# Kernel optimization log

Measured on AMD Instinct MI355X. Metric: run time of the kernel, lower is better.

Reference implementation:

```python
import jax, jax.numpy as jnp
import numpy as np

B, T, H, NH, L = 16, 1024, 256, 2, 2
NH = 4
FF = 4 * H
DT = 0.1


def _ln(x, g, b, eps=1e-5):
    m = x.mean(-1, keepdims=True)
    v = ((x - m) ** 2).mean(-1, keepdims=True)
    return (x - m) * jax.lax.rsqrt(v + eps) * g + b


def setup_inputs() -> dict:
    key = jax.random.key(0)
    ks = jax.random.split(key, 16)
    def g(i, shape, s=0.05):
        return jax.random.normal(ks[i], shape, jnp.float32) * s
    return {
        "x": jax.random.normal(ks[0], (B, T, 1), jnp.float32),
        # input projection: Linear(1->H) + LayerNorm
        "W_in": g(1, (H, 1), 0.5), "b_in": jnp.zeros(H, jnp.float32),
        "ln_in_g": jnp.ones(H, jnp.float32), "ln_in_b": jnp.zeros(H, jnp.float32),
        # LiquidODECell
        "W_x": g(2, (H, H)), "b_x": jnp.zeros(H, jnp.float32),
        "tau": jnp.ones(H, jnp.float32), "W_rec": g(3, (H, H)),
        # transformer layers (stacked over L)
        "Wqkv": g(4, (L, 3 * H, H)), "bqkv": jnp.zeros((L, 3 * H), jnp.float32),
        "Wo": g(5, (L, H, H)), "bo": jnp.zeros((L, H), jnp.float32),
        "ln1_g": jnp.ones((L, H), jnp.float32), "ln1_b": jnp.zeros((L, H), jnp.float32),
        "W1": g(6, (L, FF, H)), "b1": jnp.zeros((L, FF), jnp.float32),
        "W2": g(7, (L, H, FF)), "b2": jnp.zeros((L, H), jnp.float32),
        "ln2_g": jnp.ones((L, H), jnp.float32), "ln2_b": jnp.zeros((L, H), jnp.float32),
        # output head
        "W_fc": g(8, (1, H)), "b_fc": jnp.zeros(1, jnp.float32),
    }


def reference(x, W_in, b_in, ln_in_g, ln_in_b, W_x, b_x, tau, W_rec,
              Wqkv, bqkv, Wo, bo, ln1_g, ln1_b, W1, b1, W2, b2, ln2_g, ln2_b,
              W_fc, b_fc):
    # input proj: Linear -> LayerNorm -> GELU (exact erf gelu, matches nn.GELU)
    u = jax.nn.gelu(_ln(x @ W_in.T + b_in, ln_in_g, ln_in_b), approximate=False)  # (B,T,H)
    # LNN frontend: precompute per-step input projection, scan Euler updates
    ip = u @ W_x.T + b_x  # (B,T,H)
    def step(h, ip_t):
        f = jnp.tanh(ip_t + h @ W_rec)
        h_new = jnp.clip(h + (-h / tau + f) * DT, -10.0, 10.0)
        return h_new, h_new
    h0 = jnp.zeros((x.shape[0], H), x.dtype)
    _, states = jax.lax.scan(step, h0, jnp.swapaxes(ip, 0, 1))  # (T,B,H)
    seq = jnp.swapaxes(states, 0, 1)  # (B,T,H); dropout = identity (eval)
    dh = H // NH
    scale = 1.0 / jnp.sqrt(jnp.float32(dh))
    for l in range(L):
        qkv = seq @ Wqkv[l].T + bqkv[l]  # (B,T,3H)
        q, k, v = jnp.split(qkv, 3, axis=-1)
        def heads(t):  # (B,T,H) -> (B,NH,T,dh)
            return t.reshape(t.shape[0], t.shape[1], NH, dh).transpose(0, 2, 1, 3)
        q, k, v = heads(q), heads(k), heads(v)
        scores = jnp.einsum('bhqd,bhkd->bhqk', q, k) * scale
        attn = jax.nn.softmax(scores, axis=-1)
        ctx = jnp.einsum('bhqk,bhkd->bhqd', attn, v)  # (B,NH,T,dh)
        ctx = ctx.transpose(0, 2, 1, 3).reshape(seq.shape)
        seq = _ln(seq + ctx @ Wo[l].T + bo[l], ln1_g[l], ln1_b[l])  # post-norm
        ff = jax.nn.gelu(seq @ W1[l].T + b1[l], approximate=False) @ W2[l].T + b2[l]
        seq = _ln(seq + ff, ln2_g[l], ln2_b[l])
    pooled = seq.mean(axis=1)  # pool='mean'
    return pooled @ W_fc.T + b_fc  # (B,1)
```

## Files before the change

### kernel.cpp

```cpp
#include <hip/hip_runtime.h>
#include <math.h>


typedef unsigned short u16;
typedef __attribute__((ext_vector_type(4))) float f32x4;
typedef __attribute__((ext_vector_type(8))) short s16x8;
typedef __attribute__((ext_vector_type(4))) unsigned short u16x4;
typedef __attribute__((ext_vector_type(8))) unsigned short u16x8;

#define DEV static __device__ __forceinline__

DEV u16 f2bf_cvt(float f){
  float r; asm("v_cvt_pk_bf16_f32 %0, %1, %1" : "=v"(r) : "v"(f));
  return (u16)(__float_as_uint(r)&0xFFFFu);
}

DEV f32x4 mfma16(s16x8 a, s16x8 b, f32x4 c){
  return __builtin_amdgcn_mfma_f32_16x16x32_bf16(a,b,c,0,0,0);
}

DEV float wave_sum64(float v){
  #pragma unroll
  for(int o=1;o<64;o<<=1) v += __shfl_xor(v,o,64);
  return v;
}

DEV float geluf(float x){ return 0.5f*x*(1.f+erff(x*0.70710678118654752f)); }

DEV size_t tadr(int r, int k, int KT){
  return ((size_t)((r>>4)*KT + (k>>5)))*512 + (((k>>3)&3)*16 + (r&15))*8 + (k&7);
}

#define WB_WX   0
#define WB_WQKV 65536
#define WB_WO   458752
#define WB_W1   589824
#define WB_W2   1114112

__global__ __launch_bounds__(256) void k_wconv(const float* __restrict__ wx,
    const float* __restrict__ wqkv, const float* __restrict__ wo,
    const float* __restrict__ w1, const float* __restrict__ w2,
    u16* __restrict__ out){
  int g = blockIdx.x*4 + (threadIdx.x>>6);
  int la = threadIdx.x & 63;
  const float* src; int tl, ob, KL=3;
  if(g<128)      {src=wx;          tl=g;      ob=WB_WX;}
  else if(g<512) {src=wqkv;        tl=g-128;  ob=WB_WQKV;}
  else if(g<896) {src=wqkv+196608; tl=g-512;  ob=262144;}
  else if(g<1024){src=wo;          tl=g-896;  ob=WB_WO;}
  else if(g<1152){src=wo+65536;    tl=g-1024; ob=524288;}
  else if(g<1664){src=w1;          tl=g-1152; ob=WB_W1;}
  else if(g<2176){src=w1+262144;   tl=g-1664; ob=851968;}
  else if(g<2688){src=w2;          tl=g-2176; ob=WB_W2;   KL=5;}
  else           {src=w2+262144;   tl=g-2688; ob=1376256; KL=5;}
  int KT = 1<<KL; int K = KT*32;
  int tr = tl>>KL, tk = tl&(KT-1);
  const float* p = src + (size_t)(tr*16 + (la&15))*K + tk*32 + (la>>4)*8;
  f32x4 v0=*(const f32x4*)p, v1=*(const f32x4*)(p+4);
  s16x8 o;
  #pragma unroll
  for(int j=0;j<4;++j){ o[j]=(short)f2bf_cvt(v0[j]); o[j+4]=(short)f2bf_cvt(v1[j]); }
  *(s16x8*)(out + (size_t)ob + (size_t)tl*512 + la*8) = o;
}

__global__ __launch_bounds__(256) void k_input(const float* __restrict__ x,
    const float* __restrict__ W_in, const float* __restrict__ b_in,
    const float* __restrict__ g, const float* __restrict__ bt,
    u16* __restrict__ uout){
  int tid=threadIdx.x; int w=tid>>6; int la=tid&63;
  int tok = blockIdx.x*4 + w;
  float xv = x[(tok&15)*1024 + (tok>>4)];
  f32x4 wv = *(const f32x4*)(W_in + la*4);
  f32x4 bv = *(const f32x4*)(b_in + la*4);
  float v[4]; float s=0.f;
  #pragma unroll
  for(int j=0;j<4;++j){ v[j]=xv*wv[j]+bv[j]; s+=v[j]; }
  s = wave_sum64(s);
  float m = s*(1.f/256.f);
  float ss=0.f;
  #pragma unroll
  for(int j=0;j<4;++j){ v[j]-=m; ss+=v[j]*v[j]; }
  ss = wave_sum64(ss);
  float rs = rsqrtf(ss*(1.f/256.f)+1e-5f);
  f32x4 gv=*(const f32x4*)(g+la*4), tv=*(const f32x4*)(bt+la*4);
  u16x4 o;
  #pragma unroll
  for(int j=0;j<4;++j){ float y=v[j]*rs*gv[j]+tv[j]; o[j]=f2bf_cvt(geluf(y)); }
  int off = ((tok>>4)*8 + (la>>3))*512 + (((la>>1)&3)*16 + (tok&15))*8 + (la&1)*4;
  *(u16x4*)(uout + off) = o;
}

template<int EPI, int K>
__global__ __launch_bounds__(256) void k_gemm(const u16* __restrict__ A,
    const u16* __restrict__ W, const float* __restrict__ bias,
    const float* __restrict__ res, float* __restrict__ oF,
    u16* __restrict__ o0, u16* __restrict__ o1, u16* __restrict__ o2){
  constexpr int KT = K/32;
  int tid=threadIdx.x; int w=tid>>6; int wr=w>>1, wc=w&1;
  int la=tid&63, lq=la>>4, lr=la&15;
  int rb=blockIdx.x*128+wr*64, cb=blockIdx.y*128+wc*64;
  f32x4 acc[4][4];
  #pragma unroll
  for(int mt=0;mt<4;++mt)
    #pragma unroll
    for(int nt=0;nt<4;++nt) acc[mt][nt]=f32x4{0.f,0.f,0.f,0.f};
  const u16* Ap = A + (size_t)(rb>>4)*KT*512 + la*8;
  const u16* Wp = W + (size_t)(cb>>4)*KT*512 + la*8;
  #pragma unroll 8
  for(int kk=0;kk<KT;++kk){
    s16x8 aF[4], bF[4];
    #pragma unroll
    for(int mt=0;mt<4;++mt) aF[mt]=*(const s16x8*)(Ap + (size_t)(mt*KT+kk)*512);
    #pragma unroll
    for(int nt=0;nt<4;++nt) bF[nt]=*(const s16x8*)(Wp + (size_t)(nt*KT+kk)*512);
    #pragma unroll
    for(int mt=0;mt<4;++mt)
      #pragma unroll
      for(int nt=0;nt<4;++nt) acc[mt][nt]=mfma16(aF[mt],bF[nt],acc[mt][nt]);
  }
  #pragma unroll
  for(int mt=0;mt<4;++mt){
    #pragma unroll
    for(int nt=0;nt<4;++nt){
      int col = cb+nt*16+lr;
      float bv = bias[col];
      #pragma unroll
      for(int i=0;i<4;++i){
        int row = rb+mt*16+lq*4+i;
        float v = acc[mt][nt][i]+bv;
        if constexpr(EPI==0){
          oF[(size_t)row*256+col]=v;
        } else if constexpr(EPI==1){
          int sec=col>>8; int hcol=col&255; int head=hcol>>6, d=hcol&63;
          int t=row>>4, b=row&15, bh=b*4+head;
          u16 q=f2bf_cvt(v);
          if(sec==2){
            o2[(size_t)bh*65536 + (size_t)t*64 + d]=q;
          } else {
            size_t adr=(size_t)bh*65536 + tadr(t,d,2);
            (sec? o1 : o0)[adr]=q;
          }
        } else if constexpr(EPI==2){
          size_t adr=(size_t)row*256+col;
          oF[adr]=v+res[adr];
        } else {
          o0[tadr(row,col,32)]=f2bf_cvt(geluf(v));
        }
      }
    }
  }
}

__global__ __launch_bounds__(512) void k_scan(const float* __restrict__ ip,
    const float* __restrict__ W_rec, const float* __restrict__ tau,
    float* __restrict__ seqF){
  __shared__ u16 hbuf[2][4096];
  int tid=threadIdx.x, w=tid>>6, la=tid&63, lq=la>>4, lr=la&15;
  for(int i=tid;i<8192;i+=512) ((u16*)hbuf)[i]=0;
  int col[2]; float aC[2];
  s16x8 bF[2][8];
  #pragma unroll
  for(int nt=0;nt<2;++nt){
    int c = w*32+nt*16+lr; col[nt]=c;
    aC[nt] = 1.f - 0.1f/tau[c];
    for(int kk=0;kk<8;++kk){
      s16x8 f;
      #pragma unroll
      for(int j=0;j<8;++j){ int k=kk*32+lq*8+j; f[j]=(short)f2bf_cvt(W_rec[(size_t)k*256+c]); }
      bF[nt][kk]=f;
    }
  }
  float hC[2][4]={{0,0,0,0},{0,0,0,0}};
  const float* ipb = ip + lq*1024 + col[0];
  float* sp = seqF + lq*1024 + col[0];
  float ipc[2][4], ip1[2][4];
  #pragma unroll
  for(int nt=0;nt<2;++nt)
    #pragma unroll
    for(int i=0;i<4;++i){ ipc[nt][i]=ipb[i*256+nt*16]; ip1[nt][i]=ipb[4096+i*256+nt*16]; }
  __syncthreads();
  #pragma unroll 2
  for(int t=0;t<1024;++t){
    const char* rbuf = (const char*)hbuf + (t&1)*8192;
    char* wbuf = (char*)hbuf + ((t+1)&1)*8192;
    s16x8 aF[8];
    #pragma unroll
    for(int kk=0;kk<8;++kk){
      int off = (lr*512 + kk*64 + lq*16) ^ ((lr&7)<<4);
      aF[kk]=*(const s16x8*)(rbuf+off);
    }
    int tn = (t<1022)? t+2 : 1023;
    const float* ipp = ipb + (size_t)tn*4096;
    float ipn[2][4];
    #pragma unroll
    for(int nt=0;nt<2;++nt)
      #pragma unroll
      for(int i=0;i<4;++i) ipn[nt][i]=ipp[i*256+nt*16];
    f32x4 p0={0.f,0.f,0.f,0.f},p1={0.f,0.f,0.f,0.f};
    f32x4 q0={0.f,0.f,0.f,0.f},q1={0.f,0.f,0.f,0.f};
    #pragma unroll
    for(int kk=0;kk<4;++kk){
      p0=mfma16(aF[2*kk],  bF[0][2*kk],  p0);
      p1=mfma16(aF[2*kk+1],bF[0][2*kk+1],p1);
      q0=mfma16(aF[2*kk],  bF[1][2*kk],  q0);
      q1=mfma16(aF[2*kk+1],bF[1][2*kk+1],q1);
    }
    #pragma unroll
    for(int nt=0;nt<2;++nt){
      #pragma unroll
      for(int i=0;i<4;++i){
        float am = nt ? (q0[i]+q1[i]) : (p0[i]+p1[i]);
        float s = ipc[nt][i]+am;
        float e = __expf(2.f*s);
        float f = __builtin_fmaf(-2.f, __builtin_amdgcn_rcpf(e+1.f), 1.f);
        float hn = __builtin_fmaf(0.1f, f, aC[nt]*hC[nt][i]);
        hn = __builtin_amdgcn_fmed3f(hn,-10.f,10.f);
        hC[nt][i]=hn;
        sp[i*256+nt*16]=hn;
        u16 hb=f2bf_cvt(hn);
        int b = lq*4+i;
        int woff = (b*512 + col[nt]*2) ^ ((b&7)<<4);
        *(u16*)(wbuf+woff)=hb;
        ipc[nt][i]=ip1[nt][i];
        ip1[nt][i]=ipn[nt][i];
      }
    }
    sp += 4096;
    asm volatile("s_waitcnt lgkmcnt(0)\n\ts_barrier" ::: "memory");
  }
}

__global__ __launch_bounds__(256) void k_cvt(const float* __restrict__ in,
    u16* __restrict__ out){
  int tid=threadIdx.x; int tr=blockIdx.x; int tk=tid>>5;
  int tok0=tr*16;
  #pragma unroll
  for(int rep=0;rep<2;++rep){
    int la=(tid&31)+rep*32;
    const float* p = in + (size_t)(tok0+(la&15))*256 + tk*32 + (la>>4)*8;
    f32x4 v0=*(const f32x4*)p, v1=*(const f32x4*)(p+4);
    s16x8 o;
    #pragma unroll
    for(int j=0;j<4;++j){ o[j]=(short)f2bf_cvt(v0[j]); o[j+4]=(short)f2bf_cvt(v1[j]); }
    *(s16x8*)(out + ((size_t)tr*8+tk)*512 + la*8) = o;
  }
}

__global__ __launch_bounds__(256) void k_vt(const u16* __restrict__ V, u16* __restrict__ VT){
  __shared__ u16 tile[128][66];
  int tid=threadIdx.x; int bh=blockIdx.y, tc=blockIdx.x;
  const u16* Vb = V + (size_t)bh*65536 + (size_t)tc*128*64;
  #pragma unroll
  for(int r=0;r<4;++r){
    int t=(tid>>3)+r*32, d0=(tid&7)*8;
    *(u16x8*)&tile[t][d0] = *(const u16x8*)(Vb + t*64 + d0);
  }
  __syncthreads();
  u16* O = VT + (size_t)bh*65536 + (size_t)tc*4*512;
  #pragma unroll
  for(int wi=0;wi<4;++wi){
    int ti = (tid>>6) + wi*4;
    int tr = ti&3, tkl = ti>>2;
    int la2 = tid&63;
    int trow = tkl*32 + (la2>>4)*8;
    int d = tr*16 + (la2&15);
    u16x8 o;
    #pragma unroll
    for(int j=0;j<8;++j) o[j]=tile[trow+j][d];
    *(u16x8*)(O + (size_t)tr*32*512 + (size_t)tkl*512 + la2*8) = o;
  }
}

__global__ __launch_bounds__(256) void k_attn(const u16* __restrict__ Q,
    const u16* __restrict__ K, const u16* __restrict__ VT, u16* __restrict__ ctx){
  __shared__ u16 pbuf[4][1024];
  int tid=threadIdx.x, w=tid>>6, la=tid&63, lq=la>>4, lr=la&15;
  int bh=blockIdx.y, qb=blockIdx.x;
  char* pwc = (char*)pbuf + w*2048;
  const u16* Qbh = Q + (size_t)bh*65536;
  const u16* Kbh = K + (size_t)bh*65536;
  const u16* Vbh = VT + (size_t)bh*65536;
  int trq = qb*4 + w;
  s16x8 qF0=*(const s16x8*)(Qbh + (size_t)(trq*2  )*512 + la*8);
  s16x8 qF1=*(const s16x8*)(Qbh + (size_t)(trq*2+1)*512 + la*8);
  f32x4 O[4];
  #pragma unroll
  for(int nt=0;nt<4;++nt) O[nt]=f32x4{0.f,0.f,0.f,0.f};
  float m_run=-1e30f, l_run=0.f;
  for(int kvb=0;kvb<16;++kvb){
    f32x4 sa[4];
    #pragma unroll
    for(int mt=0;mt<4;++mt){
      int trk = kvb*4+mt;
      s16x8 k0=*(const s16x8*)(Kbh + (size_t)(trk*2  )*512 + la*8);
      s16x8 k1=*(const s16x8*)(Kbh + (size_t)(trk*2+1)*512 + la*8);
      f32x4 a=f32x4{0.f,0.f,0.f,0.f};
      a=mfma16(k0,qF0,a); a=mfma16(k1,qF1,a);
      sa[mt]=a;
    }
    float p[4][4]; float pm=-1e30f;
    #pragma unroll
    for(int mt=0;mt<4;++mt)
      #pragma unroll
      for(int i=0;i<4;++i){ p[mt][i]=sa[mt][i]*0.125f; pm=fmaxf(pm,p[mt][i]); }
    pm=fmaxf(pm,__shfl_xor(pm,16,64));
    pm=fmaxf(pm,__shfl_xor(pm,32,64));
    float mnew=fmaxf(m_run,pm);
    float c=__expf(m_run-mnew);
    float ps=0.f;
    #pragma unroll
    for(int mt=0;mt<4;++mt)
      #pragma unroll
      for(int i=0;i<4;++i){ p[mt][i]=__expf(p[mt][i]-mnew); ps+=p[mt][i]; }
    ps+=__shfl_xor(ps,16,64);
    ps+=__shfl_xor(ps,32,64);
    l_run=l_run*c+ps; m_run=mnew;
    #pragma unroll
    for(int i=0;i<4;++i){
      float ci=__shfl(c, lq*4+i, 64);
      #pragma unroll
      for(int nt=0;nt<4;++nt) O[nt][i]*=ci;
    }
    #pragma unroll
    for(int mt=0;mt<4;++mt){
      u16x4 pk;
      #pragma unroll
      for(int i=0;i<4;++i) pk[i]=f2bf_cvt(p[mt][i]);
      int off = (lr*128 + mt*32 + lq*8) ^ ((lr&7)<<4);
      *(u16x4*)(pwc+off)=pk;
    }
    #pragma unroll
    for(int kk2=0;kk2<2;++kk2){
      int off = (lr*128 + kk2*64 + lq*16) ^ ((lr&7)<<4);
      s16x8 pA = *(const s16x8*)(pwc+off);
      #pragma unroll
      for(int nt=0;nt<4;++nt){
        s16x8 vF = *(const s16x8*)(Vbh + (size_t)(nt*32 + kvb*2 + kk2)*512 + la*8);
        O[nt]=mfma16(pA, vF, O[nt]);
      }
    }
  }
  int b=bh>>2, head=bh&3;
  #pragma unroll
  for(int i=0;i<4;++i){
    float li=__shfl(l_run, lq*4+i, 64);
    float inv=1.f/li;
    int t = qb*64 + w*16 + lq*4 + i;
    int tok = t*16 + b;
    #pragma unroll
    for(int nt=0;nt<4;++nt){
      int colc = head*64 + nt*16 + lr;
      ctx[tadr(tok,colc,8)] = f2bf_cvt(O[nt][i]*inv);
    }
  }
}

__global__ __launch_bounds__(256) void k_ln(const float* __restrict__ in,
    const float* __restrict__ g, const float* __restrict__ bt,
    float* __restrict__ outF, u16* __restrict__ outB){
  int tid=threadIdx.x; int w=tid>>6; int la=tid&63;
  int tr=blockIdx.x;
  f32x4 gv=*(const f32x4*)(g+la*4), tv=*(const f32x4*)(bt+la*4);
  #pragma unroll
  for(int it=0;it<4;++it){
    int tok = tr*16 + w*4 + it;
    f32x4 v = *(const f32x4*)(in + (size_t)tok*256 + la*4);
    float s=v[0]+v[1]+v[2]+v[3];
    s=wave_sum64(s);
    float m=s*(1.f/256.f);
    float ss=0.f;
    #pragma unroll
    for(int j=0;j<4;++j){ v[j]-=m; ss+=v[j]*v[j]; }
    ss=wave_sum64(ss);
    float rs=rsqrtf(ss*(1.f/256.f)+1e-5f);
    f32x4 o; u16x4 ob;
    #pragma unroll
    for(int j=0;j<4;++j){ o[j]=v[j]*rs*gv[j]+tv[j]; ob[j]=f2bf_cvt(o[j]); }
    *(f32x4*)(outF + (size_t)tok*256 + la*4)=o;
    int off = (tr*8 + (la>>3))*512 + (((la>>1)&3)*16 + (tok&15))*8 + (la&1)*4;
    *(u16x4*)(outB+off)=ob;
  }
}

__global__ __launch_bounds__(256) void k_pool(const float* __restrict__ seqF,
    const float* __restrict__ W_fc, const float* __restrict__ b_fc,
    float* __restrict__ out){
  int tid=threadIdx.x; int b=blockIdx.y; int t0=blockIdx.x*128;
  float s=0.f;
  for(int tt=0;tt<128;++tt) s += seqF[(size_t)((t0+tt)*16 + b)*256 + tid];
  float v = s * W_fc[tid];
  v = wave_sum64(v);
  __shared__ float red[4];
  if((tid&63)==0) red[tid>>6]=v;
  __syncthreads();
  if(tid==0){
    float tot=red[0]+red[1]+red[2]+red[3];
    atomicAdd(out+b, tot*(1.f/1024.f));
    if(blockIdx.x==0) atomicAdd(out+b, b_fc[0]);
  }
}

extern "C" void kernel_launch(void* const* d_in, const int* in_sizes, int n_in,
                              void* d_out, int out_size, void* d_ws, size_t ws_size,
                              hipStream_t stream){
  const float* x      =(const float*)d_in[0];
  const float* W_in   =(const float*)d_in[1];
  const float* b_in   =(const float*)d_in[2];
  const float* ln_in_g=(const float*)d_in[3];
  const float* ln_in_b=(const float*)d_in[4];
  const float* W_x    =(const float*)d_in[5];
  const float* b_x    =(const float*)d_in[6];
  const float* tau    =(const float*)d_in[7];
  const float* W_rec  =(const float*)d_in[8];
  const float* Wqkv   =(const float*)d_in[9];
  const float* bqkv   =(const float*)d_in[10];
  const float* Wo     =(const float*)d_in[11];
  const float* bo     =(const float*)d_in[12];
  const float* ln1_g  =(const float*)d_in[13];
  const float* ln1_b  =(const float*)d_in[14];
  const float* W1     =(const float*)d_in[15];
  const float* b1     =(const float*)d_in[16];
  const float* W2     =(const float*)d_in[17];
  const float* b2     =(const float*)d_in[18];
  const float* ln2_g  =(const float*)d_in[19];
  const float* ln2_b  =(const float*)d_in[20];
  const float* W_fc   =(const float*)d_in[21];
  const float* b_fc   =(const float*)d_in[22];
  float* out=(float*)d_out;

  char* ws=(char*)d_ws;
  const size_t MB=1ull<<20;
  float* ip   =(float*)(ws);
  float* rawO = ip;
  float* seqF =(float*)(ws+16*MB);
  u16*   seqB =(u16*)  (ws+32*MB);
  u16*   Qb   =(u16*)  (ws+40*MB);
  u16*   Kb   =(u16*)  (ws+48*MB);
  u16*   Vb   =(u16*)  (ws+56*MB);
  u16*   VTb  =(u16*)  (ws+64*MB);
  u16*   ff1  =(u16*)  (ws+40*MB);
  u16*   ctx  =(u16*)  (ws+72*MB);
  u16*   wb   =(u16*)  (ws+80*MB);

  hipMemsetAsync(d_out, 0, 16*sizeof(float), stream);
  k_wconv<<<800, 256, 0, stream>>>(W_x, Wqkv, Wo, W1, W2, wb);
  k_input<<<4096, 256, 0, stream>>>(x, W_in, b_in, ln_in_g, ln_in_b, seqB);
  k_gemm<0,256><<<dim3(128,2), 256, 0, stream>>>(seqB, wb+WB_WX, b_x, nullptr, ip, nullptr, nullptr, nullptr);
  k_scan<<<1, 512, 0, stream>>>(ip, W_rec, tau, seqF);
  k_cvt <<<1024, 256, 0, stream>>>(seqF, seqB);

  for(int ly=0; ly<2; ++ly){
    k_gemm<1,256><<<dim3(128,6), 256, 0, stream>>>(seqB, wb+WB_WQKV+ly*196608, bqkv+ly*768, nullptr, nullptr, Qb, Kb, Vb);
    k_vt  <<<dim3(8,64), 256, 0, stream>>>(Vb, VTb);
    k_attn<<<dim3(16,64), 256, 0, stream>>>(Qb, Kb, VTb, ctx);
    k_gemm<2,256><<<dim3(128,2), 256, 0, stream>>>(ctx, wb+WB_WO+ly*65536, bo+ly*256, seqF, rawO, nullptr, nullptr, nullptr);
    k_ln  <<<1024, 256, 0, stream>>>(rawO, ln1_g+ly*256, ln1_b+ly*256, seqF, seqB);
    k_gemm<3,256><<<dim3(128,8), 256, 0, stream>>>(seqB, wb+WB_W1+ly*262144, b1+ly*1024, nullptr, nullptr, ff1, nullptr, nullptr);
    k_gemm<2,1024><<<dim3(128,2), 256, 0, stream>>>(ff1, wb+WB_W2+ly*262144, b2+ly*256, seqF, rawO, nullptr, nullptr, nullptr);
    k_ln  <<<1024, 256, 0, stream>>>(rawO, ln2_g+ly*256, ln2_b+ly*256, seqF, seqB);
  }
  k_pool<<<dim3(8,16), 256, 0, stream>>>(seqF, W_fc, b_fc, out);
}
```

Baseline: 1.226 ms.

## Halve scan block to 4 waves with 64 columns per wave

```diff
diff --git a/kernel.cpp b/kernel.cpp
--- a/kernel.cpp
+++ b/kernel.cpp
@@ -151,17 +151,17 @@
   }
 }
 
-__global__ __launch_bounds__(512) void k_scan(const float* __restrict__ ip,
+__global__ __launch_bounds__(256) void k_scan(const float* __restrict__ ip,
     const float* __restrict__ W_rec, const float* __restrict__ tau,
     float* __restrict__ seqF){
   __shared__ u16 hbuf[2][4096];
   int tid=threadIdx.x, w=tid>>6, la=tid&63, lq=la>>4, lr=la&15;
-  for(int i=tid;i<8192;i+=512) ((u16*)hbuf)[i]=0;
-  int col[2]; float aC[2];
-  s16x8 bF[2][8];
-  #pragma unroll
-  for(int nt=0;nt<2;++nt){
-    int c = w*32+nt*16+lr; col[nt]=c;
+  for(int i=tid;i<8192;i+=256) ((u16*)hbuf)[i]=0;
+  int col[4]; float aC[4];
+  s16x8 bF[4][8];
+  #pragma unroll
+  for(int nt=0;nt<4;++nt){
+    int c = w*64+nt*16+lr; col[nt]=c;
     aC[nt] = 1.f - 0.1f/tau[c];
     for(int kk=0;kk<8;++kk){
       s16x8 f;
@@ -170,16 +170,15 @@
       bF[nt][kk]=f;
     }
   }
-  float hC[2][4]={{0,0,0,0},{0,0,0,0}};
-  const float* ipb = ip + lq*1024 + col[0];
-  float* sp = seqF + lq*1024 + col[0];
-  float ipc[2][4], ip1[2][4];
-  #pragma unroll
-  for(int nt=0;nt<2;++nt)
-    #pragma unroll
-    for(int i=0;i<4;++i){ ipc[nt][i]=ipb[i*256+nt*16]; ip1[nt][i]=ipb[4096+i*256+nt*16]; }
+  float hC[4][4]={{0,0,0,0},{0,0,0,0},{0,0,0,0},{0,0,0,0}};
+  const float* ipb = ip + lq*1024 + w*64 + lr;
+  float* sp = seqF + lq*1024 + w*64 + lr;
+  float ipc[4][4], ipn[4][4];
+  #pragma unroll
+  for(int nt=0;nt<4;++nt)
+    #pragma unroll
+    for(int i=0;i<4;++i) ipc[nt][i]=ipb[i*256+nt*16];
   __syncthreads();
-  #pragma unroll 2
   for(int t=0;t<1024;++t){
     const char* rbuf = (const char*)hbuf + (t&1)*8192;
     char* wbuf = (char*)hbuf + ((t+1)&1)*8192;
@@ -189,40 +188,34 @@
       int off = (lr*512 + kk*64 + lq*16) ^ ((lr&7)<<4);
       aF[kk]=*(const s16x8*)(rbuf+off);
     }
-    int tn = (t<1022)? t+2 : 1023;
+    int tn = (t<1023)? t+1 : 1023;
     const float* ipp = ipb + (size_t)tn*4096;
-    float ipn[2][4];
-    #pragma unroll
-    for(int nt=0;nt<2;++nt)
+    #pragma unroll
+    for(int nt=0;nt<4;++nt)
       #pragma unroll
       for(int i=0;i<4;++i) ipn[nt][i]=ipp[i*256+nt*16];
-    f32x4 p0={0.f,0.f,0.f,0.f},p1={0.f,0.f,0.f,0.f};
-    f32x4 q0={0.f,0.f,0.f,0.f},q1={0.f,0.f,0.f,0.f};
-    #pragma unroll
-    for(int kk=0;kk<4;++kk){
-      p0=mfma16(aF[2*kk],  bF[0][2*kk],  p0);
-      p1=mfma16(aF[2*kk+1],bF[0][2*kk+1],p1);
-      q0=mfma16(aF[2*kk],  bF[1][2*kk],  q0);
-      q1=mfma16(aF[2*kk+1],bF[1][2*kk+1],q1);
-    }
-    #pragma unroll
-    for(int nt=0;nt<2;++nt){
+    f32x4 acc[4];
+    #pragma unroll
+    for(int ct=0;ct<4;++ct) acc[ct]=f32x4{0.f,0.f,0.f,0.f};
+    #pragma unroll
+    for(int kk=0;kk<8;++kk)
+      #pragma unroll
+      for(int ct=0;ct<4;++ct) acc[ct]=mfma16(aF[kk],bF[ct][kk],acc[ct]);
+    #pragma unroll
+    for(int nt=0;nt<4;++nt){
       #pragma unroll
       for(int i=0;i<4;++i){
-        float am = nt ? (q0[i]+q1[i]) : (p0[i]+p1[i]);
-        float s = ipc[nt][i]+am;
+        float s = ipc[nt][i]+acc[nt][i];
         float e = __expf(2.f*s);
         float f = __builtin_fmaf(-2.f, __builtin_amdgcn_rcpf(e+1.f), 1.f);
         float hn = __builtin_fmaf(0.1f, f, aC[nt]*hC[nt][i]);
         hn = __builtin_amdgcn_fmed3f(hn,-10.f,10.f);
         hC[nt][i]=hn;
         sp[i*256+nt*16]=hn;
-        u16 hb=f2bf_cvt(hn);
         int b = lq*4+i;
         int woff = (b*512 + col[nt]*2) ^ ((b&7)<<4);
-        *(u16*)(wbuf+woff)=hb;
-        ipc[nt][i]=ip1[nt][i];
-        ip1[nt][i]=ipn[nt][i];
+        *(u16*)(wbuf+woff)=f2bf_cvt(hn);
+        ipc[nt][i]=ipn[nt][i];
       }
     }
     sp += 4096;
@@ -446,7 +439,7 @@
   k_wconv<<<800, 256, 0, stream>>>(W_x, Wqkv, Wo, W1, W2, wb);
   k_input<<<4096, 256, 0, stream>>>(x, W_in, b_in, ln_in_g, ln_in_b, seqB);
   k_gemm<0,256><<<dim3(128,2), 256, 0, stream>>>(seqB, wb+WB_WX, b_x, nullptr, ip, nullptr, nullptr, nullptr);
-  k_scan<<<1, 512, 0, stream>>>(ip, W_rec, tau, seqF);
+  k_scan<<<1, 256, 0, stream>>>(ip, W_rec, tau, seqF);
   k_cvt <<<1024, 256, 0, stream>>>(seqF, seqB);
 
   for(int ly=0; ly<2; ++ly){
```

Result: slower. 1.518 ms (+23.9%).
